# Kernel optimization log

Hardware: AMD Instinct MI355X
Metric: run time of the kernel (lower is better)

Reference implementation:

```python
import jax, jax.numpy as jnp
import numpy as np

K = 20
EPS = 1e-5
NEG_SLOPE = 0.2


def _bn(x, g, b, m, v, axis):
    # inference batchnorm over channel axis
    shape = [1] * x.ndim
    shape[axis] = -1
    inv = g * jax.lax.rsqrt(v + EPS)
    return x * inv.reshape(shape) + (b - m * inv).reshape(shape)


def _lrelu(x):
    return jnp.where(x >= 0, x, NEG_SLOPE * x)


def _graph_feature(x, k):
    # x: (B, C, N) -> (B, 2C, N, k)
    B, C, N = x.shape
    xt = jnp.swapaxes(x, 1, 2)                      # (B, N, C)
    inner = -2.0 * jnp.einsum('bnc,bmc->bnm', xt, xt)
    xx = jnp.sum(xt * xt, axis=-1)                  # (B, N)
    pairwise = -xx[:, :, None] - inner - xx[:, None, :]  # (B, N, N) = -||xi-xj||^2
    _, idx = jax.lax.top_k(pairwise, k)             # (B, N, k)
    # gather neighbor features: (B, N, k, C)
    neigh = jnp.take_along_axis(xt[:, None, :, :], idx[:, :, :, None], axis=2)
    center = xt[:, :, None, :]                      # (B, N, 1, C)
    feat = jnp.concatenate([neigh - center, jnp.broadcast_to(center, neigh.shape)], axis=-1)
    return jnp.transpose(feat, (0, 3, 1, 2))        # (B, 2C, N, k)


def setup_inputs() -> dict:
    key = jax.random.key(0)
    ks = jax.random.split(key, 24)
    B, C, N = 8, 64, 4096
    d = {
        'x': jax.random.normal(ks[0], (B, C, N), jnp.float32),
        'w_k1': jax.random.normal(ks[1], (64, 128), jnp.float32) * 0.05,
        'g_k1': jax.random.uniform(ks[2], (64,), jnp.float32),
        'b_k1': jax.random.normal(ks[3], (64,), jnp.float32) * 0.05,
        'm_k1': jax.random.normal(ks[4], (64,), jnp.float32) * 0.05,
        'v_k1': jax.random.uniform(ks[5], (64,), jnp.float32) + 0.5,
        'w_k2': jax.random.normal(ks[6], (64, 64), jnp.float32) * 0.05,
        'g_k2': jax.random.uniform(ks[7], (64,), jnp.float32),
        'b_k2': jax.random.normal(ks[8], (64,), jnp.float32) * 0.05,
        'm_k2': jax.random.normal(ks[9], (64,), jnp.float32) * 0.05,
        'v_k2': jax.random.uniform(ks[10], (64,), jnp.float32) + 0.5,
        'w1': jax.random.normal(ks[11], (256, 64), jnp.float32) * 0.05,
        'g1': jax.random.uniform(ks[12], (256,), jnp.float32),
        'b1': jax.random.normal(ks[13], (256,), jnp.float32) * 0.05,
        'm1': jax.random.normal(ks[14], (256,), jnp.float32) * 0.05,
        'v1': jax.random.uniform(ks[15], (256,), jnp.float32) + 0.5,
        'w2': jax.random.normal(ks[16], (128, 256), jnp.float32) * 0.05,
        'g2': jax.random.uniform(ks[17], (128,), jnp.float32),
        'b2': jax.random.normal(ks[18], (128,), jnp.float32) * 0.05,
        'm2': jax.random.normal(ks[19], (128,), jnp.float32) * 0.05,
        'v2': jax.random.uniform(ks[20], (128,), jnp.float32) + 0.5,
        'w3': jax.random.normal(ks[21], (1, 128), jnp.float32) * 0.05,
        'b3': jax.random.normal(ks[22], (1,), jnp.float32) * 0.05,
    }
    return d


def reference(x, w_k1, g_k1, b_k1, m_k1, v_k1, w_k2, g_k2, b_k2, m_k2, v_k2,
              w1, g1, b1, m1, v1, w2, g2, b2, m2, v2, w3, b3):
    # kNN edge features: (B, 2C, N, k)
    f = _graph_feature(x, K)
    # EdgeConv blocks: 1x1 conv2d (bias=False) + BN + LeakyReLU
    f = _lrelu(_bn(jnp.einsum('oc,bcnk->bonk', w_k1, f), g_k1, b_k1, m_k1, v_k1, 1))
    f = _lrelu(_bn(jnp.einsum('oc,bcnk->bonk', w_k2, f), g_k2, b_k2, m_k2, v_k2, 1))
    h = jnp.max(f, axis=-1)                         # (B, 64, N) amax over neighbors
    h = _lrelu(_bn(jnp.einsum('oc,bcn->bon', w1, h), g1, b1, m1, v1, 1))
    h = _lrelu(_bn(jnp.einsum('oc,bcn->bon', w2, h), g2, b2, m2, v2, 1))
    # dropout is identity in eval mode
    out = jnp.einsum('oc,bcn->bon', w3, h) + b3[None, :, None]  # (B, 1, N)
    return out.squeeze(axis=-2)                     # (B, N)
```

## Files before the change

kernel.cpp:

```cpp
#include <hip/hip_runtime.h>
#include <hip/hip_bf16.h>

#define B_ 8
#define C_ 64
#define N_ 4096
#define K_ 20
#define EPS_ 1e-5f
#define SLOPE_ 0.2f

typedef __attribute__((ext_vector_type(8))) short bf16x8;
typedef __attribute__((ext_vector_type(4))) float f32x4;

__device__ __forceinline__ float lrelu(float x) { return x >= 0.f ? x : SLOPE_ * x; }
__device__ __forceinline__ float bf2f(unsigned short u) {
    return __uint_as_float(((unsigned int)u) << 16);
}
__device__ __forceinline__ unsigned short f2bf(float f) {
    unsigned int u = __float_as_uint(f);
    return (unsigned short)((u + 0x7FFFu + ((u >> 16) & 1u)) >> 16);
}

__device__ __forceinline__ float rdlanef(float x, int l) {
    return __int_as_float(__builtin_amdgcn_readlane(__float_as_int(x), l));
}

__global__ void __launch_bounds__(256) k_pre(const float* __restrict__ x,
                                             const float* __restrict__ wk1,
                                             float* __restrict__ yA,
                                             float* __restrict__ dd,
                                             float* __restrict__ xx,
                                             unsigned short* __restrict__ xps) {
    __shared__ float w[64][128];
    __shared__ float xs[64][64];
    int t = threadIdx.x;
    int blk = blockIdx.x;
    int b = blk >> 6;
    int n0 = (blk & 63) << 6;

    for (int i = 0; i < 8; ++i) {
        int j = i * 256 + t;
        float4 v = ((const float4*)wk1)[j];
        int o = j >> 5;
        int c4 = (j & 31) << 2;
        w[o][c4 + 0] = v.x; w[o][c4 + 1] = v.y;
        w[o][c4 + 2] = v.z; w[o][c4 + 3] = v.w;
    }
    const float* xb = x + (size_t)b * C_ * N_;
    for (int i = 0; i < 4; ++i) {
        int j = i * 256 + t;
        int c = j >> 4;
        int p4 = (j & 15) << 2;
        float4 v = *(const float4*)(xb + c * N_ + n0 + p4);
        xs[c][p4 + 0] = v.x; xs[c][p4 + 1] = v.y;
        xs[c][p4 + 2] = v.z; xs[c][p4 + 3] = v.w;
    }
    __syncthreads();

    if (t < 64) {
        float s = 0.f;
        for (int c = 0; c < 64; ++c) { float xv = xs[c][t]; s += xv * xv; }
        xx[b * N_ + n0 + t] = s;
    }

    {
        unsigned short* xc = xps + ((size_t)(b * 64 + (blk & 63))) * 8192;
#pragma unroll
        for (int q = 0; q < 2; ++q) {
            int i = q * 256 + t;
            int nl = i >> 3, oct = i & 7;
            bf16x8 hv, lv8;
#pragma unroll
            for (int j = 0; j < 8; ++j) {
                float v = xs[oct * 8 + j][nl];
                unsigned short hh = f2bf(v);
                hv[j] = (short)hh;
                lv8[j] = (short)f2bf(v - bf2f(hh));
            }
            int unit = oct ^ (nl & 7);
            *(bf16x8*)&xc[nl * 64 + unit * 8] = hv;
            *(bf16x8*)&xc[4096 + nl * 64 + unit * 8] = lv8;
        }
    }

    int p = t & 63, og = t >> 6;
    for (int oi = 0; oi < 16; ++oi) {
        int o = og * 16 + oi;
        float sA = 0.f, sB = 0.f;
        for (int c = 0; c < 64; ++c) {
            float xv = xs[c][p];
            sA += w[o][c] * xv;
            sB += w[o][64 + c] * xv;
        }
        size_t base = ((size_t)(b * N_ + n0 + p)) * 64 + o;
        yA[base] = sA;
        dd[base] = sB - sA;
    }
}

__global__ void __launch_bounds__(512) k_topk(const unsigned short* __restrict__ xps,
                                              const float* __restrict__ xx,
                                              int* __restrict__ idxg) {
    __shared__ float sc[2][32][68];
    int t = threadIdx.x;
    int lane = t & 63;
    int w = t >> 6;
    int wr = w >> 2;
    int wc = w & 3;
    int blk = blockIdx.x;
    int b = blk >> 7;
    int n0 = (blk & 127) << 5;
    int bc = b << 6;
    const float* xxb = xx + b * N_;
    int pa = ((lane + 1) & 63) << 2;

    const unsigned short* xcA = xps + ((size_t)(bc + ((blk & 127) >> 1))) * 8192;
    int anl = ((blk & 1) << 5) + (wr << 4) + (lane & 15);
    bf16x8 ah[2], al[2];
#pragma unroll
    for (int kc = 0; kc < 2; ++kc) {
        int unit = (kc * 4 + (lane >> 4)) ^ (anl & 7);
        ah[kc] = *(const bf16x8*)&xcA[anl * 64 + unit * 8];
        al[kc] = *(const bf16x8*)&xcA[4096 + anl * 64 + unit * 8];
    }

    int n_ = (wc << 4) + (lane & 15);
    int off0 = n_ * 64 + (((lane >> 4)) ^ (n_ & 7)) * 8;
    int off1 = n_ * 64 + ((4 + (lane >> 4)) ^ (n_ & 7)) * 8;

    float lv[4];
    int   li[4];
#pragma unroll
    for (int i = 0; i < 4; ++i) { lv[i] = -3.0e38f; li[i] = 0; }

    auto ins = [&](float& lvr, int& lir, float s, int m0) {
        float mnc = rdlanef(lvr, 19);
        unsigned long long mask = __ballot(s > mnc);
        while (mask) {
            int j = (int)__builtin_ctzll(mask);
            mask &= mask - 1;
            float sv = rdlanef(s, j);
            if (sv > mnc) {
                unsigned long long gt = __ballot(lane < 20 && lvr > sv);
                int cpos = __popcll(gt);
                float upv = __int_as_float(
                    __builtin_amdgcn_ds_permute(pa, __float_as_int(lvr)));
                int   upi = __builtin_amdgcn_ds_permute(pa, lir);
                if (lane >= cpos && lane < 20) {
                    lvr = (lane == cpos) ? sv : upv;
                    lir = (lane == cpos) ? (m0 + j) : upi;
                }
                mnc = rdlanef(lvr, 19);
            }
        }
    };

    const unsigned short* xcB = xps + (size_t)bc * 8192;
    bf16x8 bh0 = *(const bf16x8*)&xcB[off0];
    bf16x8 bl0 = *(const bf16x8*)&xcB[4096 + off0];
    bf16x8 bh1 = *(const bf16x8*)&xcB[off1];
    bf16x8 bl1 = *(const bf16x8*)&xcB[4096 + off1];
    float xxv = xxb[n_];

    for (int mc = 0; mc < 64; ++mc) {
        f32x4 acc = {0.f, 0.f, 0.f, 0.f};
        acc = __builtin_amdgcn_mfma_f32_16x16x32_bf16(ah[0], bh0, acc, 0, 0, 0);
        acc = __builtin_amdgcn_mfma_f32_16x16x32_bf16(ah[0], bl0, acc, 0, 0, 0);
        acc = __builtin_amdgcn_mfma_f32_16x16x32_bf16(al[0], bh0, acc, 0, 0, 0);
        acc = __builtin_amdgcn_mfma_f32_16x16x32_bf16(al[0], bl0, acc, 0, 0, 0);
        acc = __builtin_amdgcn_mfma_f32_16x16x32_bf16(ah[1], bh1, acc, 0, 0, 0);
        acc = __builtin_amdgcn_mfma_f32_16x16x32_bf16(ah[1], bl1, acc, 0, 0, 0);
        acc = __builtin_amdgcn_mfma_f32_16x16x32_bf16(al[1], bh1, acc, 0, 0, 0);
        acc = __builtin_amdgcn_mfma_f32_16x16x32_bf16(al[1], bl1, acc, 0, 0, 0);

#pragma unroll
        for (int r = 0; r < 4; ++r)
            sc[mc & 1][(wr << 4) + ((lane >> 4) << 2) + r][n_] = 2.f * acc[r] - xxv;

        if (mc + 1 < 64) {
            const unsigned short* xn2 = xps + (size_t)(bc + mc + 1) * 8192;
            bh0 = *(const bf16x8*)&xn2[off0];
            bl0 = *(const bf16x8*)&xn2[4096 + off0];
            bh1 = *(const bf16x8*)&xn2[off1];
            bl1 = *(const bf16x8*)&xn2[4096 + off1];
            xxv = xxb[((mc + 1) << 6) + n_];
        }

        if (mc > 0) {
            int m0p = (mc - 1) << 6;
#pragma unroll
            for (int i = 0; i < 4; ++i) {
                int lrow = (w << 2) + i;
                float s = sc[(mc - 1) & 1][lrow][lane];
                ins(lv[i], li[i], s, m0p);
            }
        }
        __syncthreads();
    }

    {
        int m0p = 63 << 6;
#pragma unroll
        for (int i = 0; i < 4; ++i) {
            int lrow = (w << 2) + i;
            float s = sc[1][lrow][lane];
            ins(lv[i], li[i], s, m0p);
        }
    }

#pragma unroll
    for (int i = 0; i < 4; ++i) {
        int n = n0 + (w << 2) + i;
        if (lane < K_)
            idxg[((size_t)(b * N_ + n)) * K_ + lane] = li[i];
    }
}

__global__ void __launch_bounds__(256) k_edge(const float* __restrict__ yA,
                                              const float* __restrict__ dd,
                                              const int* __restrict__ idxg,
                                              const float* __restrict__ wk2,
                                              const float* __restrict__ g1,
                                              const float* __restrict__ bb1,
                                              const float* __restrict__ mm1,
                                              const float* __restrict__ vv1,
                                              const float* __restrict__ g2,
                                              const float* __restrict__ bb2,
                                              const float* __restrict__ mm2,
                                              const float* __restrict__ vv2,
                                              float* __restrict__ ht) {
    __shared__ unsigned short wimg[8192];
    __shared__ float ubuf[64 * 164];
    __shared__ float s1c[64], t1c[64], s2c[64], t2c[64];
    __shared__ float ddl[8][64];
    __shared__ int   il[8][K_];
    __shared__ float hl[8][64];
    unsigned short* timgH = (unsigned short*)ubuf;
    unsigned short* timgL = timgH + 160 * 64;
    float* ct = ubuf;

    int t = threadIdx.x;
    int lane = t & 63;
    int w = t >> 6;
    int blk = blockIdx.x;
    int b = blk >> 9;
    int n0 = (blk & 511) << 3;

    for (int rep = 0; rep < 2; ++rep) {
        int i = rep * 256 + t;
        int row = i >> 3, oct = i & 7;
        float4 wa = *(const float4*)(wk2 + row * 64 + oct * 8);
        float4 wb = *(const float4*)(wk2 + row * 64 + oct * 8 + 4);
        float wv[8] = {wa.x, wa.y, wa.z, wa.w, wb.x, wb.y, wb.z, wb.w};
        bf16x8 hv, lv8;
#pragma unroll
        for (int j = 0; j < 8; ++j) {
            unsigned short hh = f2bf(wv[j]);
            hv[j] = (short)hh;
            lv8[j] = (short)f2bf(wv[j] - bf2f(hh));
        }
        int unit = oct ^ (row & 7);
        *(bf16x8*)&wimg[row * 64 + unit * 8] = hv;
        *(bf16x8*)&wimg[4096 + row * 64 + unit * 8] = lv8;
    }
    if (t < 64) {
        float g = g1[t], be = bb1[t], m = mm1[t], v = vv1[t];
        float s = g * rsqrtf(v + EPS_);
        s1c[t] = s; t1c[t] = be - m * s;
        g = g2[t]; be = bb2[t]; m = mm2[t]; v = vv2[t];
        s = g * rsqrtf(v + EPS_);
        s2c[t] = s; t2c[t] = be - m * s;
    }
    size_t pbase = (size_t)(b * N_ + n0);
    for (int i = t; i < 512; i += 256) {
        int pt = i >> 6, o = i & 63;
        ddl[pt][o] = dd[(pbase + pt) * 64 + o];
    }
    if (t < 8 * K_) {
        int pt = t / K_, k = t % K_;
        il[pt][k] = idxg[(pbase + pt) * K_ + k];
    }
    __syncthreads();

    const float* yAb = yA + (size_t)(b * N_) * 64;
    float4 ga[5][2];
    int gcol[5], goct[5], gpt[5];
#pragma unroll
    for (int rep = 0; rep < 5; ++rep) {
        int j = rep * 256 + t;
        int pt = j / 160;
        int r = j - pt * 160;
        int k = r >> 3, oct = r & 7;
        int m = il[pt][k];
        const float* src = yAb + (size_t)m * 64 + oct * 8;
        ga[rep][0] = *(const float4*)src;
        ga[rep][1] = *(const float4*)(src + 4);
        gcol[rep] = pt * 20 + k; goct[rep] = oct; gpt[rep] = pt;
    }
#pragma unroll
    for (int rep = 0; rep < 5; ++rep) {
        int oct = goct[rep], pt = gpt[rep], col = gcol[rep];
        float yv[8] = {ga[rep][0].x, ga[rep][0].y, ga[rep][0].z, ga[rep][0].w,
                       ga[rep][1].x, ga[rep][1].y, ga[rep][1].z, ga[rep][1].w};
        bf16x8 hv, lv8;
#pragma unroll
        for (int jj = 0; jj < 8; ++jj) {
            int oc = oct * 8 + jj;
            float v = lrelu(s1c[oc] * (yv[jj] + ddl[pt][oc]) + t1c[oc]);
            unsigned short hh = f2bf(v);
            hv[jj] = (short)hh;
            lv8[jj] = (short)f2bf(v - bf2f(hh));
        }
        int unit = oct ^ (col & 7);
        *(bf16x8*)&timgH[col * 64 + unit * 8] = hv;
        *(bf16x8*)&timgL[col * 64 + unit * 8] = lv8;
    }
    __syncthreads();

    int anl = (w << 4) + (lane & 15);
    bf16x8 ah[2], al[2];
#pragma unroll
    for (int kc = 0; kc < 2; ++kc) {
        int unit = (kc * 4 + (lane >> 4)) ^ (anl & 7);
        ah[kc] = *(const bf16x8*)&wimg[anl * 64 + unit * 8];
        al[kc] = *(const bf16x8*)&wimg[4096 + anl * 64 + unit * 8];
    }
    f32x4 acc[10];
#pragma unroll
    for (int nt = 0; nt < 10; ++nt) {
        int col = nt * 16 + (lane & 15);
        int u0 = ((lane >> 4)) ^ (col & 7);
        int u1 = (4 + (lane >> 4)) ^ (col & 7);
        bf16x8 bh0 = *(const bf16x8*)&timgH[col * 64 + u0 * 8];
        bf16x8 bl0 = *(const bf16x8*)&timgL[col * 64 + u0 * 8];
        bf16x8 bh1 = *(const bf16x8*)&timgH[col * 64 + u1 * 8];
        bf16x8 bl1 = *(const bf16x8*)&timgL[col * 64 + u1 * 8];
        f32x4 a = {0.f, 0.f, 0.f, 0.f};
        a = __builtin_amdgcn_mfma_f32_16x16x32_bf16(ah[0], bh0, a, 0, 0, 0);
        a = __builtin_amdgcn_mfma_f32_16x16x32_bf16(ah[0], bl0, a, 0, 0, 0);
        a = __builtin_amdgcn_mfma_f32_16x16x32_bf16(al[0], bh0, a, 0, 0, 0);
        a = __builtin_amdgcn_mfma_f32_16x16x32_bf16(al[0], bl0, a, 0, 0, 0);
        a = __builtin_amdgcn_mfma_f32_16x16x32_bf16(ah[1], bh1, a, 0, 0, 0);
        a = __builtin_amdgcn_mfma_f32_16x16x32_bf16(ah[1], bl1, a, 0, 0, 0);
        a = __builtin_amdgcn_mfma_f32_16x16x32_bf16(al[1], bh1, a, 0, 0, 0);
        a = __builtin_amdgcn_mfma_f32_16x16x32_bf16(al[1], bl1, a, 0, 0, 0);
        acc[nt] = a;
    }
    __syncthreads();

#pragma unroll
    for (int nt = 0; nt < 10; ++nt) {
#pragma unroll
        for (int r = 0; r < 4; ++r)
            ct[((w << 4) + ((lane >> 4) << 2) + r) * 164 + nt * 16 + (lane & 15)] =
                acc[nt][r];
    }
    __syncthreads();

#pragma unroll
    for (int rep = 0; rep < 2; ++rep) {
        int pair = rep * 256 + t;
        int o2 = pair >> 3, pt = pair & 7;
        const float* row = &ct[o2 * 164 + pt * 20];
        float4 c0 = *(const float4*)(row + 0);
        float4 c1 = *(const float4*)(row + 4);
        float4 c2 = *(const float4*)(row + 8);
        float4 c3 = *(const float4*)(row + 12);
        float4 c4 = *(const float4*)(row + 16);
        float mx = fmaxf(fmaxf(fmaxf(c0.x, c0.y), fmaxf(c0.z, c0.w)),
                   fmaxf(fmaxf(fmaxf(c1.x, c1.y), fmaxf(c1.z, c1.w)),
                   fmaxf(fmaxf(fmaxf(c2.x, c2.y), fmaxf(c2.z, c2.w)),
                   fmaxf(fmaxf(fmaxf(c3.x, c3.y), fmaxf(c3.z, c3.w)),
                         fmaxf(fmaxf(c4.x, c4.y), fmaxf(c4.z, c4.w))))));
        hl[pt][o2] = lrelu(s2c[o2] * mx + t2c[o2]);
    }
    __syncthreads();

    float* htb = ht + (size_t)b * 64 * N_;
    for (int i = t; i < 512; i += 256) {
        int o = i >> 3, pt2 = i & 7;
        htb[o * N_ + n0 + pt2] = hl[pt2][o];
    }
}

__global__ void __launch_bounds__(256) k_head(const float* __restrict__ ht,
                                              const float* __restrict__ w1,
                                              const float* __restrict__ g1,
                                              const float* __restrict__ bb1,
                                              const float* __restrict__ mm1,
                                              const float* __restrict__ vv1,
                                              const float* __restrict__ w2,
                                              const float* __restrict__ g2,
                                              const float* __restrict__ bb2,
                                              const float* __restrict__ mm2,
                                              const float* __restrict__ vv2,
                                              const float* __restrict__ w3,
                                              const float* __restrict__ b3,
                                              float* __restrict__ out) {
    __shared__ float hbuf[64][64];
    __shared__ float a1[256][64];
    __shared__ float a2[128][64];
    __shared__ float sA[256], tA[256], sB[128], tB[128];
    int t = threadIdx.x;
    int blk = blockIdx.x;
    int b = blk >> 6;
    int n0 = (blk & 63) << 6;
    const float* htb = ht + (size_t)b * 64 * N_;

    for (int i = 0; i < 16; ++i) {
        int j = i * 256 + t;
        int o = j >> 6, pt = j & 63;
        hbuf[o][pt] = htb[o * N_ + n0 + pt];
    }
    {
        float g = g1[t], be = bb1[t], m = mm1[t], v = vv1[t];
        float s = g * rsqrtf(v + EPS_);
        sA[t] = s; tA[t] = be - m * s;
    }
    if (t < 128) {
        float g = g2[t], be = bb2[t], m = mm2[t], v = vv2[t];
        float s = g * rsqrtf(v + EPS_);
        sB[t] = s; tB[t] = be - m * s;
    }
    __syncthreads();

    int ptg = t & 15, rg = t >> 4;
    int pt4 = ptg << 2;

    for (int ib = 0; ib < 4; ++ib) {
        int r0 = (rg << 4) + (ib << 2);
        float acc[4][4] = {};
        for (int o4 = 0; o4 < 16; ++o4) {
            float hf[4][4];
            for (int c = 0; c < 4; ++c) {
                float4 q = *(const float4*)&hbuf[(o4 << 2) + c][pt4];
                hf[c][0] = q.x; hf[c][1] = q.y; hf[c][2] = q.z; hf[c][3] = q.w;
            }
            for (int j = 0; j < 4; ++j) {
                float4 wv4 = *(const float4*)(w1 + (r0 + j) * 64 + (o4 << 2));
                float wv[4] = {wv4.x, wv4.y, wv4.z, wv4.w};
                for (int c = 0; c < 4; ++c)
                    for (int pp = 0; pp < 4; ++pp)
                        acc[j][pp] += wv[c] * hf[c][pp];
            }
        }
        for (int j = 0; j < 4; ++j) {
            int r = r0 + j;
            float4 ov;
            ov.x = lrelu(sA[r] * acc[j][0] + tA[r]);
            ov.y = lrelu(sA[r] * acc[j][1] + tA[r]);
            ov.z = lrelu(sA[r] * acc[j][2] + tA[r]);
            ov.w = lrelu(sA[r] * acc[j][3] + tA[r]);
            *(float4*)&a1[r][pt4] = ov;
        }
    }
    __syncthreads();

    for (int ib = 0; ib < 2; ++ib) {
        int r0 = (rg << 3) + (ib << 2);
        float acc[4][4] = {};
        for (int p4i = 0; p4i < 64; ++p4i) {
            float af[4][4];
            for (int c = 0; c < 4; ++c) {
                float4 q = *(const float4*)&a1[(p4i << 2) + c][pt4];
                af[c][0] = q.x; af[c][1] = q.y; af[c][2] = q.z; af[c][3] = q.w;
            }
            for (int j = 0; j < 4; ++j) {
                float4 wv4 = *(const float4*)(w2 + (r0 + j) * 256 + (p4i << 2));
                float wv[4] = {wv4.x, wv4.y, wv4.z, wv4.w};
                for (int c = 0; c < 4; ++c)
                    for (int pp = 0; pp < 4; ++pp)
                        acc[j][pp] += wv[c] * af[c][pp];
            }
        }
        for (int j = 0; j < 4; ++j) {
            int r = r0 + j;
            float4 ov;
            ov.x = lrelu(sB[r] * acc[j][0] + tB[r]);
            ov.y = lrelu(sB[r] * acc[j][1] + tB[r]);
            ov.z = lrelu(sB[r] * acc[j][2] + tB[r]);
            ov.w = lrelu(sB[r] * acc[j][3] + tB[r]);
            *(float4*)&a2[r][pt4] = ov;
        }
    }
    __syncthreads();

    if (t < 64) {
        float accv = 0.f;
        for (int q = 0; q < 128; ++q) accv += w3[q] * a2[q][t];
        accv += b3[0];
        out[b * N_ + n0 + t] = accv;
    }
}

extern "C" void kernel_launch(void* const* d_in, const int* in_sizes, int n_in,
                              void* d_out, int out_size, void* d_ws, size_t ws_size,
                              hipStream_t stream) {
    (void)in_sizes; (void)n_in; (void)out_size; (void)ws_size;
    const float* x    = (const float*)d_in[0];
    const float* wk1  = (const float*)d_in[1];
    const float* gk1  = (const float*)d_in[2];
    const float* bk1  = (const float*)d_in[3];
    const float* mk1  = (const float*)d_in[4];
    const float* vk1  = (const float*)d_in[5];
    const float* wk2  = (const float*)d_in[6];
    const float* gk2  = (const float*)d_in[7];
    const float* bk2  = (const float*)d_in[8];
    const float* mk2  = (const float*)d_in[9];
    const float* vk2  = (const float*)d_in[10];
    const float* w1   = (const float*)d_in[11];
    const float* g1   = (const float*)d_in[12];
    const float* b1   = (const float*)d_in[13];
    const float* m1   = (const float*)d_in[14];
    const float* v1   = (const float*)d_in[15];
    const float* w2   = (const float*)d_in[16];
    const float* g2   = (const float*)d_in[17];
    const float* b2   = (const float*)d_in[18];
    const float* m2   = (const float*)d_in[19];
    const float* v2   = (const float*)d_in[20];
    const float* w3   = (const float*)d_in[21];
    const float* b3   = (const float*)d_in[22];

    char* ws = (char*)d_ws;
    float* yA  = (float*)(ws);
    float* dd  = (float*)(ws + 8388608);
    float* xx  = (float*)(ws + 16777216);
    int*   idx = (int*)  (ws + 16908288);
    float* ht  = (float*)(ws + 19529728);
    unsigned short* xps = (unsigned short*)(ws + 27918336);

    k_pre <<<B_ * (N_ / 64), 256, 0, stream>>>(x, wk1, yA, dd, xx, xps);
    k_topk<<<B_ * (N_ / 32), 512, 0, stream>>>(xps, xx, idx);
    k_edge<<<B_ * (N_ / 8),  256, 0, stream>>>(yA, dd, idx, wk2,
                                               gk1, bk1, mk1, vk1,
                                               gk2, bk2, mk2, vk2, ht);
    k_head<<<B_ * (N_ / 64), 256, 0, stream>>>(ht, w1, g1, b1, m1, v1,
                                               w2, g2, b2, m2, v2, w3, b3,
                                               (float*)d_out);
}
```

Baseline: 357.7 us.

## Compute first edge-conv projection with split-bf16 MFMA and simplify top-k insert

The k_pre kernel now converts wk1 and the x tile into swizzled hi/lo bf16 images in shared memory. It computes the yA and dd projections with 16x16x32 bf16 MFMA instructions instead of a scalar FMA loop over shared memory, and writes the results as float4. Using all four hi/lo cross terms keeps accuracy close to fp32, at the cost of more shared memory and an extra barrier. The top-k insertion loop also drops the per-candidate recheck against the current minimum and the refresh of that minimum. Candidates that no longer qualify then compute a position of 20 and change nothing, which saves a readlane and a branch but adds ballot and permute work for such candidates.

```diff
diff --git a/kernel.cpp b/kernel.cpp
--- a/kernel.cpp
+++ b/kernel.cpp
@@ -30,21 +30,16 @@
                                              float* __restrict__ dd,
                                              float* __restrict__ xx,
                                              unsigned short* __restrict__ xps) {
-    __shared__ float w[64][128];
     __shared__ float xs[64][64];
+    __shared__ unsigned short wimg[16384];
+    __shared__ unsigned short ximg[8192];
     int t = threadIdx.x;
+    int lane = t & 63;
+    int w = t >> 6;
     int blk = blockIdx.x;
     int b = blk >> 6;
     int n0 = (blk & 63) << 6;
 
-    for (int i = 0; i < 8; ++i) {
-        int j = i * 256 + t;
-        float4 v = ((const float4*)wk1)[j];
-        int o = j >> 5;
-        int c4 = (j & 31) << 2;
-        w[o][c4 + 0] = v.x; w[o][c4 + 1] = v.y;
-        w[o][c4 + 2] = v.z; w[o][c4 + 3] = v.w;
-    }
     const float* xb = x + (size_t)b * C_ * N_;
     for (int i = 0; i < 4; ++i) {
         int j = i * 256 + t;
@@ -54,6 +49,24 @@
         xs[c][p4 + 0] = v.x; xs[c][p4 + 1] = v.y;
         xs[c][p4 + 2] = v.z; xs[c][p4 + 3] = v.w;
     }
+    for (int rep = 0; rep < 4; ++rep) {
+        int i = rep * 256 + t;
+        int m = i >> 3, oct = i & 7;
+        const float* src = wk1 + (m & 63) * 128 + ((m >> 6) << 6) + oct * 8;
+        float4 a4 = *(const float4*)src;
+        float4 b4 = *(const float4*)(src + 4);
+        float wv[8] = {a4.x, a4.y, a4.z, a4.w, b4.x, b4.y, b4.z, b4.w};
+        bf16x8 hv, lv8;
+#pragma unroll
+        for (int j = 0; j < 8; ++j) {
+            unsigned short hh = f2bf(wv[j]);
+            hv[j] = (short)hh;
+            lv8[j] = (short)f2bf(wv[j] - bf2f(hh));
+        }
+        int unit = oct ^ (m & 7);
+        *(bf16x8*)&wimg[m * 64 + unit * 8] = hv;
+        *(bf16x8*)&wimg[8192 + m * 64 + unit * 8] = lv8;
+    }
     __syncthreads();
 
     if (t < 64) {
@@ -62,38 +75,73 @@
         xx[b * N_ + n0 + t] = s;
     }
 
-    {
-        unsigned short* xc = xps + ((size_t)(b * 64 + (blk & 63))) * 8192;
-#pragma unroll
-        for (int q = 0; q < 2; ++q) {
-            int i = q * 256 + t;
-            int nl = i >> 3, oct = i & 7;
-            bf16x8 hv, lv8;
-#pragma unroll
-            for (int j = 0; j < 8; ++j) {
-                float v = xs[oct * 8 + j][nl];
-                unsigned short hh = f2bf(v);
-                hv[j] = (short)hh;
-                lv8[j] = (short)f2bf(v - bf2f(hh));
-            }
-            int unit = oct ^ (nl & 7);
-            *(bf16x8*)&xc[nl * 64 + unit * 8] = hv;
-            *(bf16x8*)&xc[4096 + nl * 64 + unit * 8] = lv8;
-        }
-    }
-
-    int p = t & 63, og = t >> 6;
-    for (int oi = 0; oi < 16; ++oi) {
-        int o = og * 16 + oi;
-        float sA = 0.f, sB = 0.f;
-        for (int c = 0; c < 64; ++c) {
-            float xv = xs[c][p];
-            sA += w[o][c] * xv;
-            sB += w[o][64 + c] * xv;
-        }
-        size_t base = ((size_t)(b * N_ + n0 + p)) * 64 + o;
-        yA[base] = sA;
-        dd[base] = sB - sA;
+    unsigned short* xc = xps + ((size_t)(b * 64 + (blk & 63))) * 8192;
+#pragma unroll
+    for (int q = 0; q < 2; ++q) {
+        int i = q * 256 + t;
+        int nl = i >> 3, oct = i & 7;
+        bf16x8 hv, lv8;
+#pragma unroll
+        for (int j = 0; j < 8; ++j) {
+            float v = xs[oct * 8 + j][nl];
+            unsigned short hh = f2bf(v);
+            hv[j] = (short)hh;
+            lv8[j] = (short)f2bf(v - bf2f(hh));
+        }
+        int unit = oct ^ (nl & 7);
+        *(bf16x8*)&ximg[nl * 64 + unit * 8] = hv;
+        *(bf16x8*)&ximg[4096 + nl * 64 + unit * 8] = lv8;
+        *(bf16x8*)&xc[nl * 64 + unit * 8] = hv;
+        *(bf16x8*)&xc[4096 + nl * 64 + unit * 8] = lv8;
+    }
+    __syncthreads();
+
+    int mA = (w << 4) + (lane & 15);
+    int mB = ((w + 4) << 4) + (lane & 15);
+    bf16x8 ahA[2], alA[2], ahB[2], alB[2];
+#pragma unroll
+    for (int kc = 0; kc < 2; ++kc) {
+        int uA = (kc * 4 + (lane >> 4)) ^ (mA & 7);
+        int uB = (kc * 4 + (lane >> 4)) ^ (mB & 7);
+        ahA[kc] = *(const bf16x8*)&wimg[mA * 64 + uA * 8];
+        alA[kc] = *(const bf16x8*)&wimg[8192 + mA * 64 + uA * 8];
+        ahB[kc] = *(const bf16x8*)&wimg[mB * 64 + uB * 8];
+        alB[kc] = *(const bf16x8*)&wimg[8192 + mB * 64 + uB * 8];
+    }
+    size_t pbase = (size_t)(b * N_ + n0);
+#pragma unroll
+    for (int nt = 0; nt < 4; ++nt) {
+        int p = nt * 16 + (lane & 15);
+        int u0 = ((lane >> 4)) ^ (p & 7);
+        int u1 = (4 + (lane >> 4)) ^ (p & 7);
+        bf16x8 bh0 = *(const bf16x8*)&ximg[p * 64 + u0 * 8];
+        bf16x8 bl0 = *(const bf16x8*)&ximg[4096 + p * 64 + u0 * 8];
+        bf16x8 bh1 = *(const bf16x8*)&ximg[p * 64 + u1 * 8];
+        bf16x8 bl1 = *(const bf16x8*)&ximg[4096 + p * 64 + u1 * 8];
+        f32x4 aA = {0.f, 0.f, 0.f, 0.f};
+        aA = __builtin_amdgcn_mfma_f32_16x16x32_bf16(ahA[0], bh0, aA, 0, 0, 0);
+        aA = __builtin_amdgcn_mfma_f32_16x16x32_bf16(ahA[0], bl0, aA, 0, 0, 0);
+        aA = __builtin_amdgcn_mfma_f32_16x16x32_bf16(alA[0], bh0, aA, 0, 0, 0);
+        aA = __builtin_amdgcn_mfma_f32_16x16x32_bf16(alA[0], bl0, aA, 0, 0, 0);
+        aA = __builtin_amdgcn_mfma_f32_16x16x32_bf16(ahA[1], bh1, aA, 0, 0, 0);
+        aA = __builtin_amdgcn_mfma_f32_16x16x32_bf16(ahA[1], bl1, aA, 0, 0, 0);
+        aA = __builtin_amdgcn_mfma_f32_16x16x32_bf16(alA[1], bh1, aA, 0, 0, 0);
+        aA = __builtin_amdgcn_mfma_f32_16x16x32_bf16(alA[1], bl1, aA, 0, 0, 0);
+        f32x4 aB = {0.f, 0.f, 0.f, 0.f};
+        aB = __builtin_amdgcn_mfma_f32_16x16x32_bf16(ahB[0], bh0, aB, 0, 0, 0);
+        aB = __builtin_amdgcn_mfma_f32_16x16x32_bf16(ahB[0], bl0, aB, 0, 0, 0);
+        aB = __builtin_amdgcn_mfma_f32_16x16x32_bf16(alB[0], bh0, aB, 0, 0, 0);
+        aB = __builtin_amdgcn_mfma_f32_16x16x32_bf16(alB[0], bl0, aB, 0, 0, 0);
+        aB = __builtin_amdgcn_mfma_f32_16x16x32_bf16(ahB[1], bh1, aB, 0, 0, 0);
+        aB = __builtin_amdgcn_mfma_f32_16x16x32_bf16(ahB[1], bl1, aB, 0, 0, 0);
+        aB = __builtin_amdgcn_mfma_f32_16x16x32_bf16(alB[1], bh1, aB, 0, 0, 0);
+        aB = __builtin_amdgcn_mfma_f32_16x16x32_bf16(alB[1], bl1, aB, 0, 0, 0);
+
+        int obase = (w << 4) + ((lane >> 4) << 2);
+        float4 ya4 = {aA[0], aA[1], aA[2], aA[3]};
+        float4 dd4 = {aB[0] - aA[0], aB[1] - aA[1], aB[2] - aA[2], aB[3] - aA[3]};
+        *(float4*)(yA + (pbase + p) * 64 + obase) = ya4;
+        *(float4*)(dd + (pbase + p) * 64 + obase) = dd4;
     }
 }
 
@@ -139,17 +187,14 @@
             int j = (int)__builtin_ctzll(mask);
             mask &= mask - 1;
             float sv = rdlanef(s, j);
-            if (sv > mnc) {
-                unsigned long long gt = __ballot(lane < 20 && lvr > sv);
-                int cpos = __popcll(gt);
-                float upv = __int_as_float(
-                    __builtin_amdgcn_ds_permute(pa, __float_as_int(lvr)));
-                int   upi = __builtin_amdgcn_ds_permute(pa, lir);
-                if (lane >= cpos && lane < 20) {
-                    lvr = (lane == cpos) ? sv : upv;
-                    lir = (lane == cpos) ? (m0 + j) : upi;
-                }
-                mnc = rdlanef(lvr, 19);
+            unsigned long long gt = __ballot(lane < 20 && lvr > sv);
+            int cpos = __popcll(gt);
+            float upv = __int_as_float(
+                __builtin_amdgcn_ds_permute(pa, __float_as_int(lvr)));
+            int   upi = __builtin_amdgcn_ds_permute(pa, lir);
+            if (lane >= cpos && lane < 20) {
+                lvr = (lane == cpos) ? sv : upv;
+                lir = (lane == cpos) ? (m0 + j) : upi;
             }
         }
     };
```

Result: faster. 341.4 us (-4.6%).
